# Kernel optimization log

Measured on AMD Instinct MI355X. Metric: run time of the kernel, lower is better.

Reference implementation:

```python
import jax, jax.numpy as jnp
import numpy as np

N = 50000

def setup_inputs() -> dict:
    key = jax.random.key(0)
    ks = jax.random.split(key, 5)
    d, h, E = 128, 512, 800000
    x = jax.random.normal(ks[0], (N, d), dtype=jnp.float32)
    edge_index = jax.random.randint(ks[1], (2, E), 0, N, dtype=jnp.int32)
    eps = jnp.zeros((1, 1), dtype=jnp.float32)
    W1 = jax.random.normal(ks[2], (d, h), dtype=jnp.float32) * (1.0 / np.sqrt(d))
    b1 = jnp.zeros((h,), dtype=jnp.float32)
    W2 = jax.random.normal(ks[3], (h, d), dtype=jnp.float32) * (1.0 / np.sqrt(h))
    b2 = jnp.zeros((d,), dtype=jnp.float32)
    return {"x": x, "edge_index": edge_index, "eps": eps,
            "W1": W1, "b1": b1, "W2": W2, "b2": b2}

def reference(x, edge_index, eps, W1, b1, W2, b2):
    src, dst = edge_index[0], edge_index[1]
    # node -> edge gather (ptens edge subgraph sums both endpoints): [E, d]
    node2edge = x[src] + x[dst]
    # edge -> node gather (sum over incident edges): [N, d]
    nbr = jax.ops.segment_sum(node2edge, src, num_segments=N) + \
          jax.ops.segment_sum(node2edge, dst, num_segments=N)
    # degree correction: subtract deg_i * x_i, leaving sum of neighbor features
    ones = jnp.ones_like(src, dtype=x.dtype)
    deg = jax.ops.segment_sum(ones, src, num_segments=N) + \
          jax.ops.segment_sum(ones, dst, num_segments=N)
    neighbor = nbr - x * deg[:, None]
    # eps-scaled residual then MLP
    out = (1.0 + eps) * x + neighbor
    hmid = jax.nn.relu(out @ W1 + b1)
    return hmid @ W2 + b2
```

## Files before the change

kernel.cpp:

```cpp
#include <hip/hip_runtime.h>

#define MROWS 32
#define FILLK 8
#define WCHUNK 4096

typedef __attribute__((ext_vector_type(8))) short short8v;
typedef __attribute__((ext_vector_type(4))) float f32x4;

__device__ __forceinline__ unsigned short f2bf(float f) {
  unsigned u = __builtin_bit_cast(unsigned, f);
  unsigned r = (u + 0x7fffu + ((u >> 16) & 1u)) >> 16;
  return (unsigned short)r;
}
__device__ __forceinline__ float bf2f(unsigned short s) {
  return __builtin_bit_cast(float, (unsigned)s << 16);
}

__global__ __launch_bounds__(256) void prep_kernel(
    const float* __restrict__ x, const float* __restrict__ W1,
    const float* __restrict__ W2, int* __restrict__ zp,
    unsigned short* __restrict__ xb, short* __restrict__ w1p,
    short* __restrict__ w2p, int N, int zn) {
  const int Z = zn;
  const int X = 16 * N;
  const int grand = Z + X + 131072;
  int i = blockIdx.x * blockDim.x + threadIdx.x;
  int stride = gridDim.x * blockDim.x;
  for (; i < grand; i += stride) {
    if (i < Z) {
      zp[i] = 0;
    } else if (i < Z + X) {
      int t = i - Z;
      const float4* p = (const float4*)(x + (size_t)t * 8);
      float4 q0 = p[0], q1 = p[1];
      short8v s;
      s[0] = (short)f2bf(q0.x); s[1] = (short)f2bf(q0.y);
      s[2] = (short)f2bf(q0.z); s[3] = (short)f2bf(q0.w);
      s[4] = (short)f2bf(q1.x); s[5] = (short)f2bf(q1.y);
      s[6] = (short)f2bf(q1.z); s[7] = (short)f2bf(q1.w);
      *(short8v*)(xb + (size_t)t * 8) = s;
    } else {
      int t = i - Z - X;
      int idx = t & 65535;
      int frag = idx >> 9, rem = idx & 511;
      int lane = rem >> 3, j = rem & 7;
      if (t < 65536) {
        int nt = frag >> 2, ks = frag & 3;
        int k = ks * 32 + (lane >> 4) * 8 + j;
        int c = nt * 16 + (lane & 15);
        w1p[idx] = (short)f2bf(W1[k * 512 + c]);
      } else {
        int nt = frag >> 4, ks = frag & 15;
        int k = ks * 32 + (lane >> 4) * 8 + j;
        int c = nt * 16 + (lane & 15);
        w2p[idx] = (short)f2bf(W2[k * 128 + c]);
      }
    }
  }
}


__global__ __launch_bounds__(256) void bcount_kernel(const int* __restrict__ ei,
    int* __restrict__ bcount, int total, int NB) {
  __shared__ int hist[512];
  for (int i = threadIdx.x; i < 512; i += 256) hist[i] = 0;
  __syncthreads();
  int i = blockIdx.x * blockDim.x + threadIdx.x;
  int stride = gridDim.x * blockDim.x;
  for (; i < total; i += stride) atomicAdd(&hist[((unsigned)ei[i]) >> 7], 1);
  __syncthreads();
  for (int b = threadIdx.x; b < NB; b += 256)
    if (hist[b]) atomicAdd(&bcount[b], hist[b]);
}

__global__ __launch_bounds__(64) void scan_cur_kernel(const int* __restrict__ bcount,
    int* __restrict__ boffs, int* __restrict__ gcursor, int n) {
  int lane = threadIdx.x;
  int carry = 0;
  if (lane == 0) boffs[0] = 0;
  for (int base = 0; base < n; base += 64) {
    int i = base + lane;
    int v0 = (i < n) ? bcount[i] : 0;
    int v = v0;
    #pragma unroll
    for (int off = 1; off < 64; off <<= 1) {
      int t = __shfl_up(v, off, 64);
      if (lane >= off) v += t;
    }
    int incl = v + carry;
    if (i < n) {
      boffs[i + 1] = incl;
      gcursor[i] = incl - v0;
    }
    carry = __shfl(incl, 63, 64);
  }
}

__global__ __launch_bounds__(256) void bwrite_kernel(const int* __restrict__ ei,
    int* __restrict__ gcursor, unsigned* __restrict__ bdata, int E, int NB) {
  __shared__ int hist[512];
  __shared__ int gbase[512];
  const int tid = threadIdx.x;
  const int total = 2 * E;
  const int base0 = blockIdx.x * WCHUNK;
  if (base0 >= total) return;
  const int cnt = min(WCHUNK, total - base0);
  for (int i = tid; i < 512; i += 256) hist[i] = 0;
  __syncthreads();
  for (int k = tid; k < cnt; k += 256)
    atomicAdd(&hist[((unsigned)ei[base0 + k]) >> 7], 1);
  __syncthreads();
  for (int b = tid; b < NB; b += 256) {
    int h = hist[b];
    gbase[b] = h ? atomicAdd(&gcursor[b], h) : 0;
  }
  __syncthreads();
  for (int i = tid; i < 512; i += 256) hist[i] = 0;
  __syncthreads();
  for (int k = tid; k < cnt; k += 256) {
    int i = base0 + k;
    int v = ei[i];
    int other = (i < E) ? ei[i + E] : ei[i - E];
    int b = ((unsigned)v) >> 7;
    int r = atomicAdd(&hist[b], 1);
    bdata[gbase[b] + r] = (((unsigned)(v & 127)) << 16) | (unsigned)other;
  }
}

__global__ __launch_bounds__(256) void bsort_kernel(const unsigned* __restrict__ bdata,
    const int* __restrict__ boffs, unsigned short* __restrict__ adj2,
    int* __restrict__ rowptr, int N, int E2) {
  __shared__ int hist[128];
  __shared__ int loff[129];
  __shared__ int cur[128];
  const int b = blockIdx.x;
  const int beg = boffs[b], end = boffs[b + 1];
  const int tid = threadIdx.x;
  if (tid < 128) hist[tid] = 0;
  __syncthreads();
  for (int p = beg + tid; p < end; p += 256)
    atomicAdd(&hist[bdata[p] >> 16], 1);
  __syncthreads();
  if (tid < 64) {
    int a0 = hist[tid], a1 = hist[tid + 64];
    int v0 = a0;
    #pragma unroll
    for (int off = 1; off < 64; off <<= 1) {
      int t = __shfl_up(v0, off, 64);
      if (tid >= off) v0 += t;
    }
    int tot0 = __shfl(v0, 63, 64);
    int v1 = a1;
    #pragma unroll
    for (int off = 1; off < 64; off <<= 1) {
      int t = __shfl_up(v1, off, 64);
      if (tid >= off) v1 += t;
    }
    loff[tid] = v0 - a0;
    loff[tid + 64] = tot0 + v1 - a1;
    cur[tid] = v0 - a0;
    cur[tid + 64] = tot0 + v1 - a1;
    int n0 = (b << 7) + tid;
    int n1 = n0 + 64;
    if (n0 < N) rowptr[n0] = beg + loff[tid];
    if (n1 < N) rowptr[n1] = beg + loff[tid + 64];
  }
  if (b == 0 && tid == 0) rowptr[N] = E2;
  __syncthreads();
  for (int p = beg + tid; p < end; p += 256) {
    unsigned e = bdata[p];
    int r = atomicAdd(&cur[e >> 16], 1);
    adj2[beg + r] = (unsigned short)(e & 0xFFFFu);
  }
}

__global__ __launch_bounds__(256) void aggb_s_kernel(const unsigned short* __restrict__ xb,
    const float* __restrict__ eps, const int* __restrict__ rowptr,
    const unsigned short* __restrict__ adj2, unsigned short* __restrict__ aggb, int N) {
  int n = blockIdx.x * 16 + (threadIdx.x >> 4);
  if (n >= N) return;
  int lane = threadIdx.x & 15;
  float s = 1.0f + eps[0];
  const unsigned short* lanebase = xb + (size_t)lane * 8;
  short8v own = *(const short8v*)(lanebase + ((size_t)n << 7));
  float accA[8], accB[8];
  #pragma unroll
  for (int j = 0; j < 8; ++j) { accA[j] = bf2f((unsigned short)own[j]) * s; accB[j] = 0.f; }
  int beg = rowptr[n], end = rowptr[n + 1];
  int p = beg;
  for (; p + 4 <= end; p += 4) {
    int j0 = adj2[p + 0];
    int j1 = adj2[p + 1];
    int j2 = adj2[p + 2];
    int j3 = adj2[p + 3];
    short8v v0 = *(const short8v*)(lanebase + ((size_t)j0 << 7));
    short8v v1 = *(const short8v*)(lanebase + ((size_t)j1 << 7));
    short8v v2 = *(const short8v*)(lanebase + ((size_t)j2 << 7));
    short8v v3 = *(const short8v*)(lanebase + ((size_t)j3 << 7));
    #pragma unroll
    for (int j = 0; j < 8; ++j) {
      accA[j] += bf2f((unsigned short)v0[j]) + bf2f((unsigned short)v2[j]);
      accB[j] += bf2f((unsigned short)v1[j]) + bf2f((unsigned short)v3[j]);
    }
  }
  for (; p < end; ++p) {
    int jn = adj2[p];
    short8v v = *(const short8v*)(lanebase + ((size_t)jn << 7));
    #pragma unroll
    for (int j = 0; j < 8; ++j) accA[j] += bf2f((unsigned short)v[j]);
  }
  short8v o;
  #pragma unroll
  for (int j = 0; j < 8; ++j) o[j] = (short)f2bf(accA[j] + accB[j]);
  *(short8v*)(aggb + ((size_t)n << 7) + lane * 8) = o;
}


__global__ __launch_bounds__(256) void count_kernel(const int* __restrict__ ei,
                                                    int* __restrict__ deg, int total) {
  int i = blockIdx.x * blockDim.x + threadIdx.x;
  int stride = gridDim.x * blockDim.x;
  for (; i < total; i += stride) atomicAdd(&deg[ei[i]], 1);
}

__global__ __launch_bounds__(64) void scan_kernel(const int* __restrict__ deg,
                                                  int* __restrict__ rowptr, int n) {
  int lane = threadIdx.x;
  int carry = 0;
  if (lane == 0) rowptr[0] = 0;
  for (int base = 0; base < n; base += 64) {
    int i = base + lane;
    int v = (i < n) ? deg[i] : 0;
    #pragma unroll
    for (int off = 1; off < 64; off <<= 1) {
      int t = __shfl_up(v, off, 64);
      if (lane >= off) v += t;
    }
    int incl = v + carry;
    if (i < n) rowptr[i + 1] = incl;
    carry = __shfl(incl, 63, 64);
  }
}

__global__ __launch_bounds__(256) void chunk_reduce_kernel(const int* __restrict__ deg,
                                                           int* __restrict__ csum, int n) {
  __shared__ int wsum[4];
  int base = blockIdx.x * 1024;
  int tid = threadIdx.x;
  int s = 0;
  #pragma unroll
  for (int j = 0; j < 4; ++j) {
    int i = base + tid * 4 + j;
    if (i < n) s += deg[i];
  }
  #pragma unroll
  for (int off = 1; off < 64; off <<= 1) s += __shfl_xor(s, off, 64);
  if ((tid & 63) == 0) wsum[tid >> 6] = s;
  __syncthreads();
  if (tid == 0) csum[blockIdx.x] = wsum[0] + wsum[1] + wsum[2] + wsum[3];
}

__global__ __launch_bounds__(256) void chunk_scan_c_kernel(const int* __restrict__ deg,
    const int* __restrict__ coffs, int* __restrict__ rowptr,
    int* __restrict__ cursor, int n) {
  __shared__ int wpart[4];
  int b = blockIdx.x;
  int base = b * 1024;
  int tid = threadIdx.x;
  int lane = tid & 63, wv = tid >> 6;
  int v[4], s = 0;
  #pragma unroll
  for (int j = 0; j < 4; ++j) {
    int i = base + tid * 4 + j;
    v[j] = (i < n) ? deg[i] : 0;
    s += v[j];
  }
  int incl = s;
  #pragma unroll
  for (int off = 1; off < 64; off <<= 1) {
    int t = __shfl_up(incl, off, 64);
    if (lane >= off) incl += t;
  }
  if (lane == 63) wpart[wv] = incl;
  __syncthreads();
  int woff = 0;
  for (int k = 0; k < wv; ++k) woff += wpart[k];
  int run = incl - s + woff + coffs[b];
  #pragma unroll
  for (int j = 0; j < 4; ++j) {
    int i = base + tid * 4 + j;
    if (i < n) {
      cursor[i] = run;
      run += v[j];
      rowptr[i + 1] = run;
    }
  }
  if (b == 0 && tid == 0) rowptr[0] = 0;
}

__global__ __launch_bounds__(256) void fill_batch_kernel(const int* __restrict__ ei,
    int* __restrict__ cursor, int* __restrict__ adj, int E) {
  int total = 2 * E;
  int T = gridDim.x * blockDim.x;
  int t = blockIdx.x * blockDim.x + threadIdx.x;
  int vv[FILLK], oo[FILLK], pp[FILLK];
  for (long long base = 0; base < total; base += (long long)T * FILLK) {
    #pragma unroll
    for (int k = 0; k < FILLK; ++k) {
      long long i = base + (long long)k * T + t;
      if (i < total) {
        int ii = (int)i;
        vv[k] = ei[ii];
        oo[k] = (ii < E) ? ei[ii + E] : ei[ii - E];
      } else {
        vv[k] = -1; oo[k] = 0;
      }
    }
    #pragma unroll
    for (int k = 0; k < FILLK; ++k)
      pp[k] = (vv[k] >= 0) ? atomicAdd(&cursor[vv[k]], 1) : 0;
    #pragma unroll
    for (int k = 0; k < FILLK; ++k)
      if (vv[k] >= 0) adj[pp[k]] = oo[k];
  }
}

__global__ __launch_bounds__(256) void aggb_kernel(const unsigned short* __restrict__ xb,
    const float* __restrict__ eps, const int* __restrict__ rowptr,
    const int* __restrict__ adj, unsigned short* __restrict__ aggb, int N) {
  int n = blockIdx.x * 16 + (threadIdx.x >> 4);
  if (n >= N) return;
  int lane = threadIdx.x & 15;
  float s = 1.0f + eps[0];
  const unsigned short* base = xb + (size_t)n * 128 + lane * 8;
  short8v own = *(const short8v*)base;
  float acc[8];
  #pragma unroll
  for (int j = 0; j < 8; ++j) acc[j] = bf2f((unsigned short)own[j]) * s;
  int beg = rowptr[n], end = rowptr[n + 1];
  for (int p = beg; p < end; ++p) {
    int nb = adj[p];
    short8v v = *(const short8v*)(xb + (size_t)nb * 128 + lane * 8);
    #pragma unroll
    for (int j = 0; j < 8; ++j) acc[j] += bf2f((unsigned short)v[j]);
  }
  short8v o;
  #pragma unroll
  for (int j = 0; j < 8; ++j) o[j] = (short)f2bf(acc[j]);
  *(short8v*)(aggb + (size_t)n * 128 + lane * 8) = o;
}


__global__ __launch_bounds__(256) void init_kernel(const float* __restrict__ x,
                                                   const float* __restrict__ eps,
                                                   float* __restrict__ agg, int total4) {
  float scale = 1.0f + eps[0];
  int idx = blockIdx.x * blockDim.x + threadIdx.x;
  int stride = gridDim.x * blockDim.x;
  const float4* x4 = (const float4*)x;
  float4* a4 = (float4*)agg;
  for (int i = idx; i < total4; i += stride) {
    float4 v = x4[i];
    v.x *= scale; v.y *= scale; v.z *= scale; v.w *= scale;
    a4[i] = v;
  }
}

__global__ __launch_bounds__(256) void scatter_kernel(const float* __restrict__ x,
    const int* __restrict__ src, const int* __restrict__ dst,
    float* __restrict__ agg, int E) {
  long long total = (long long)E * 32;
  long long idx = (long long)blockIdx.x * blockDim.x + threadIdx.x;
  long long stride = (long long)gridDim.x * blockDim.x;
  for (; idx < total; idx += stride) {
    int e = (int)(idx >> 5);
    int f4 = (int)(idx & 31);
    int s = src[e], d = dst[e];
    float4 xs = ((const float4*)x)[(size_t)s * 32 + f4];
    float4 xd = ((const float4*)x)[(size_t)d * 32 + f4];
    float* as = agg + (size_t)s * 128 + f4 * 4;
    float* ad = agg + (size_t)d * 128 + f4 * 4;
    atomicAdd(as + 0, xd.x); atomicAdd(as + 1, xd.y);
    atomicAdd(as + 2, xd.z); atomicAdd(as + 3, xd.w);
    atomicAdd(ad + 0, xs.x); atomicAdd(ad + 1, xs.y);
    atomicAdd(ad + 2, xs.z); atomicAdd(ad + 3, xs.w);
  }
}


__global__ __launch_bounds__(256) void mlp_mfma_b_kernel(
    const unsigned short* __restrict__ aggb, const short* __restrict__ w1p,
    const short* __restrict__ w2p, const float* __restrict__ b1,
    const float* __restrict__ b2, float* __restrict__ out, int N) {
  __shared__ short s_h[32 * 512];
  const int tid = threadIdx.x;
  const int w = tid >> 6, l = tid & 63;
  const int l15 = l & 15, lg = l >> 4;
  const int brow = blockIdx.x * 32;

  short8v af[2][4];
  #pragma unroll
  for (int mt = 0; mt < 2; ++mt) {
    int row = brow + mt * 16 + l15;
    #pragma unroll
    for (int ks = 0; ks < 4; ++ks) {
      short8v s = (short8v)(short)0;
      if (row < N)
        s = *(const short8v*)(aggb + (size_t)row * 128 + ks * 32 + lg * 8);
      af[mt][ks] = s;
    }
  }

  f32x4 acc1[2][8];
  #pragma unroll
  for (int nt = 0; nt < 8; ++nt) {
    float bv = b1[(w * 8 + nt) * 16 + l15];
    acc1[0][nt] = (f32x4){bv, bv, bv, bv};
    acc1[1][nt] = (f32x4){bv, bv, bv, bv};
  }
  #pragma unroll
  for (int nt = 0; nt < 8; ++nt) {
    int ntg = w * 8 + nt;
    #pragma unroll
    for (int ks = 0; ks < 4; ++ks) {
      short8v bf = *(const short8v*)(w1p + ((ntg * 4 + ks) << 9) + l * 8);
      acc1[0][nt] = __builtin_amdgcn_mfma_f32_16x16x32_bf16(af[0][ks], bf, acc1[0][nt], 0, 0, 0);
      acc1[1][nt] = __builtin_amdgcn_mfma_f32_16x16x32_bf16(af[1][ks], bf, acc1[1][nt], 0, 0, 0);
    }
  }

  #pragma unroll
  for (int mt = 0; mt < 2; ++mt)
    #pragma unroll
    for (int nt = 0; nt < 8; ++nt) {
      int col = (w * 8 + nt) * 16 + l15;
      #pragma unroll
      for (int reg = 0; reg < 4; ++reg) {
        int row = mt * 16 + lg * 4 + reg;
        float v = fmaxf(acc1[mt][nt][reg], 0.f);
        int byte = (row << 10) + (col << 1);
        byte ^= (row & 7) << 4;
        *(short*)((char*)s_h + byte) = (short)f2bf(v);
      }
    }
  __syncthreads();

  f32x4 acc2[2][2];
  #pragma unroll
  for (int ntl = 0; ntl < 2; ++ntl) {
    float bv = b2[(w * 2 + ntl) * 16 + l15];
    acc2[0][ntl] = (f32x4){bv, bv, bv, bv};
    acc2[1][ntl] = (f32x4){bv, bv, bv, bv};
  }
  #pragma unroll
  for (int ks = 0; ks < 16; ++ks) {
    short8v a2[2];
    #pragma unroll
    for (int mt = 0; mt < 2; ++mt) {
      int row = mt * 16 + l15;
      int byte = (row << 10) + ((ks * 32 + lg * 8) << 1);
      byte ^= (row & 7) << 4;
      a2[mt] = *(short8v*)((char*)s_h + byte);
    }
    #pragma unroll
    for (int ntl = 0; ntl < 2; ++ntl) {
      int ntg = w * 2 + ntl;
      short8v bf = *(const short8v*)(w2p + ((ntg * 16 + ks) << 9) + l * 8);
      acc2[0][ntl] = __builtin_amdgcn_mfma_f32_16x16x32_bf16(a2[0], bf, acc2[0][ntl], 0, 0, 0);
      acc2[1][ntl] = __builtin_amdgcn_mfma_f32_16x16x32_bf16(a2[1], bf, acc2[1][ntl], 0, 0, 0);
    }
  }

  #pragma unroll
  for (int mt = 0; mt < 2; ++mt)
    #pragma unroll
    for (int ntl = 0; ntl < 2; ++ntl)
      #pragma unroll
      for (int reg = 0; reg < 4; ++reg) {
        int row = brow + mt * 16 + lg * 4 + reg;
        if (row < N)
          out[(size_t)row * 128 + (w * 2 + ntl) * 16 + l15] = acc2[mt][ntl][reg];
      }
}


__global__ __launch_bounds__(256) void mlp_kernel(
    const float* agg, const float* __restrict__ W1,
    const float* __restrict__ b1, const float* __restrict__ W2,
    const float* __restrict__ b2, float* out, int N) {
  __shared__ float s_agg[MROWS][128];
  __shared__ float s_h[MROWS][65];
  const int tid = threadIdx.x;
  const int block_row = blockIdx.x * MROWS;

  for (int i = tid; i < MROWS * 32; i += 256) {
    int r = i >> 5, c4 = i & 31;
    if (block_row + r < N)
      ((float4*)&s_agg[r][0])[c4] = ((const float4*)agg)[(size_t)(block_row + r) * 32 + c4];
    else
      ((float4*)&s_agg[r][0])[c4] = make_float4(0.f, 0.f, 0.f, 0.f);
  }
  __syncthreads();

  const int r = tid >> 3;
  const int f0 = (tid & 7) << 4;
  float acc[16];
  #pragma unroll
  for (int j = 0; j < 16; ++j) acc[j] = b2[f0 + j];

  const int hc = tid & 63;
  const int hr0 = tid >> 6;

  for (int h0 = 0; h0 < 512; h0 += 64) {
    float sum[8];
    float bv = b1[h0 + hc];
    #pragma unroll
    for (int j = 0; j < 8; ++j) sum[j] = bv;
    const float* w1col = W1 + h0 + hc;
    #pragma unroll 4
    for (int k = 0; k < 128; ++k) {
      float wv = w1col[(size_t)k * 512];
      #pragma unroll
      for (int j = 0; j < 8; ++j) sum[j] += s_agg[hr0 + (j << 2)][k] * wv;
    }
    __syncthreads();
    #pragma unroll
    for (int j = 0; j < 8; ++j) s_h[hr0 + (j << 2)][hc] = fmaxf(sum[j], 0.f);
    __syncthreads();

    for (int hcc = 0; hcc < 64; ++hcc) {
      float hv = s_h[r][hcc];
      const float4* w2p = (const float4*)(W2 + (size_t)(h0 + hcc) * 128 + f0);
      float4 w0 = w2p[0], w1v = w2p[1], w2v = w2p[2], w3v = w2p[3];
      acc[0]  += hv * w0.x;  acc[1]  += hv * w0.y;  acc[2]  += hv * w0.z;  acc[3]  += hv * w0.w;
      acc[4]  += hv * w1v.x; acc[5]  += hv * w1v.y; acc[6]  += hv * w1v.z; acc[7]  += hv * w1v.w;
      acc[8]  += hv * w2v.x; acc[9]  += hv * w2v.y; acc[10] += hv * w2v.z; acc[11] += hv * w2v.w;
      acc[12] += hv * w3v.x; acc[13] += hv * w3v.y; acc[14] += hv * w3v.z; acc[15] += hv * w3v.w;
    }
  }

  if (block_row + r < N) {
    float4* op = (float4*)(out + (size_t)(block_row + r) * 128 + f0);
    op[0] = make_float4(acc[0],  acc[1],  acc[2],  acc[3]);
    op[1] = make_float4(acc[4],  acc[5],  acc[6],  acc[7]);
    op[2] = make_float4(acc[8],  acc[9],  acc[10], acc[11]);
    op[3] = make_float4(acc[12], acc[13], acc[14], acc[15]);
  }
}

extern "C" void kernel_launch(void* const* d_in, const int* in_sizes, int n_in,
                              void* d_out, int out_size, void* d_ws, size_t ws_size,
                              hipStream_t stream) {
  const float* x   = (const float*)d_in[0];
  const int*   ei  = (const int*)d_in[1];
  const float* eps = (const float*)d_in[2];
  const float* W1  = (const float*)d_in[3];
  const float* b1  = (const float*)d_in[4];
  const float* W2  = (const float*)d_in[5];
  const float* b2  = (const float*)d_in[6];
  float* out = (float*)d_out;

  const int N = in_sizes[0] / 128;
  const int E = in_sizes[1] / 2;
  const int nChunks = (N + 1023) / 1024;
  const int NB = (N + 127) >> 7;
  int mblocks = (N + MROWS - 1) / MROWS;

  size_t wp_bytes = 2u * 65536u * sizeof(short);
  size_t xb_bytes = ((size_t)N * 128 * sizeof(short) + 15) & ~(size_t)15;

  size_t bt_ints = (size_t)2 * NB + (NB + 1) + (size_t)(N + 1) + (size_t)2 * E + (size_t)(E + 1);
  size_t bt_al = ((bt_ints * sizeof(int)) + 15) & ~(size_t)15;
  size_t need_bt = bt_al + wp_bytes + 2 * xb_bytes;

  size_t csr_ints = (size_t)(3 * N + 1 + 2 * E) + (size_t)(2 * nChunks + 1);
  size_t csr_al = ((csr_ints * sizeof(int)) + 15) & ~(size_t)15;
  size_t need_t1 = csr_al + wp_bytes;
  size_t need_t2 = need_t1 + 2 * xb_bytes;

  if (N <= 65536 && ws_size >= need_bt) {
    int* bcount  = (int*)d_ws;
    int* gcursor = bcount + NB;
    int* boffs   = gcursor + NB;
    int* rowptr  = boffs + NB + 1;
    unsigned* bdata = (unsigned*)(rowptr + N + 1);
    unsigned short* adj2 = (unsigned short*)(bdata + 2 * E);
    short* w1p  = (short*)((char*)d_ws + bt_al);
    short* w2p  = w1p + 65536;
    unsigned short* xb   = (unsigned short*)((char*)d_ws + bt_al + wp_bytes);
    unsigned short* aggb = (unsigned short*)((char*)d_ws + bt_al + wp_bytes + xb_bytes);

    prep_kernel<<<2048, 256, 0, stream>>>(x, W1, W2, bcount, xb, w1p, w2p, N, NB);
    bcount_kernel<<<256, 256, 0, stream>>>(ei, bcount, 2 * E, NB);
    scan_cur_kernel<<<1, 64, 0, stream>>>(bcount, boffs, gcursor, NB);
    int wblocks = (2 * E + WCHUNK - 1) / WCHUNK;
    bwrite_kernel<<<wblocks, 256, 0, stream>>>(ei, gcursor, bdata, E, NB);
    bsort_kernel<<<NB, 256, 0, stream>>>(bdata, boffs, adj2, rowptr, N, 2 * E);
    aggb_s_kernel<<<(N + 15) / 16, 256, 0, stream>>>(xb, eps, rowptr, adj2, aggb, N);
    mlp_mfma_b_kernel<<<mblocks, 256, 0, stream>>>(aggb, w1p, w2p, b1, b2, out, N);
  } else if (ws_size >= need_t2) {
    int* deg    = (int*)d_ws;
    int* cursor = deg + N;
    int* rowptr = cursor + N;
    int* adj    = rowptr + (N + 1);
    int* csum   = adj + 2 * E;
    int* coffs  = csum + nChunks;
    short* w1p  = (short*)((char*)d_ws + csr_al);
    short* w2p  = w1p + 65536;
    unsigned short* xb   = (unsigned short*)((char*)d_ws + need_t1);
    unsigned short* aggb = (unsigned short*)((char*)d_ws + need_t1 + xb_bytes);

    prep_kernel<<<2048, 256, 0, stream>>>(x, W1, W2, deg, xb, w1p, w2p, N, 2 * N);
    count_kernel<<<4096, 256, 0, stream>>>(ei, deg, 2 * E);
    chunk_reduce_kernel<<<nChunks, 256, 0, stream>>>(deg, csum, N);
    scan_kernel<<<1, 64, 0, stream>>>(csum, coffs, nChunks);
    chunk_scan_c_kernel<<<nChunks, 256, 0, stream>>>(deg, coffs, rowptr, cursor, N);
    int fblocks = (2 * E + 256 * FILLK - 1) / (256 * FILLK);
    fill_batch_kernel<<<fblocks, 256, 0, stream>>>(ei, cursor, adj, E);
    aggb_kernel<<<(N + 15) / 16, 256, 0, stream>>>(xb, eps, rowptr, adj, aggb, N);
    mlp_mfma_b_kernel<<<mblocks, 256, 0, stream>>>(aggb, w1p, w2p, b1, b2, out, N);
  } else {
    init_kernel<<<2048, 256, 0, stream>>>(x, eps, out, N * 32);
    scatter_kernel<<<4096, 256, 0, stream>>>(x, ei, ei + E, out, E);
    mlp_kernel<<<mblocks, 256, 0, stream>>>(out, W1, b1, W2, b2, out, N);
  }
}
```

Baseline: 162.8 us.

## Fuse neighbor aggregation into MFMA MLP kernel via shared-memory staging

```diff
diff --git a/kernel.cpp b/kernel.cpp
--- a/kernel.cpp
+++ b/kernel.cpp
@@ -174,45 +174,151 @@
   }
 }
 
-__global__ __launch_bounds__(256) void aggb_s_kernel(const unsigned short* __restrict__ xb,
-    const float* __restrict__ eps, const int* __restrict__ rowptr,
-    const unsigned short* __restrict__ adj2, unsigned short* __restrict__ aggb, int N) {
-  int n = blockIdx.x * 16 + (threadIdx.x >> 4);
-  if (n >= N) return;
-  int lane = threadIdx.x & 15;
-  float s = 1.0f + eps[0];
-  const unsigned short* lanebase = xb + (size_t)lane * 8;
-  short8v own = *(const short8v*)(lanebase + ((size_t)n << 7));
-  float accA[8], accB[8];
-  #pragma unroll
-  for (int j = 0; j < 8; ++j) { accA[j] = bf2f((unsigned short)own[j]) * s; accB[j] = 0.f; }
-  int beg = rowptr[n], end = rowptr[n + 1];
-  int p = beg;
-  for (; p + 4 <= end; p += 4) {
-    int j0 = adj2[p + 0];
-    int j1 = adj2[p + 1];
-    int j2 = adj2[p + 2];
-    int j3 = adj2[p + 3];
-    short8v v0 = *(const short8v*)(lanebase + ((size_t)j0 << 7));
-    short8v v1 = *(const short8v*)(lanebase + ((size_t)j1 << 7));
-    short8v v2 = *(const short8v*)(lanebase + ((size_t)j2 << 7));
-    short8v v3 = *(const short8v*)(lanebase + ((size_t)j3 << 7));
-    #pragma unroll
-    for (int j = 0; j < 8; ++j) {
-      accA[j] += bf2f((unsigned short)v0[j]) + bf2f((unsigned short)v2[j]);
-      accB[j] += bf2f((unsigned short)v1[j]) + bf2f((unsigned short)v3[j]);
-    }
-  }
-  for (; p < end; ++p) {
-    int jn = adj2[p];
-    short8v v = *(const short8v*)(lanebase + ((size_t)jn << 7));
-    #pragma unroll
-    for (int j = 0; j < 8; ++j) accA[j] += bf2f((unsigned short)v[j]);
-  }
-  short8v o;
-  #pragma unroll
-  for (int j = 0; j < 8; ++j) o[j] = (short)f2bf(accA[j] + accB[j]);
-  *(short8v*)(aggb + ((size_t)n << 7) + lane * 8) = o;
+__global__ __launch_bounds__(256) void agg_mlp_fused_kernel(
+    const unsigned short* __restrict__ xb, const float* __restrict__ eps,
+    const int* __restrict__ rowptr, const unsigned short* __restrict__ adj2,
+    const short* __restrict__ w1p, const short* __restrict__ w2p,
+    const float* __restrict__ b1, const float* __restrict__ b2,
+    float* __restrict__ out, int N) {
+  __shared__ short s_agg[32 * 128];
+  __shared__ short s_h[32 * 512];
+  const int tid = threadIdx.x;
+  const int brow = blockIdx.x * 32;
+
+  {
+    const int lane16 = tid & 15;
+    const unsigned short* lanebase = xb + (size_t)lane16 * 8;
+    float s = 1.0f + eps[0];
+    #pragma unroll
+    for (int half = 0; half < 2; ++half) {
+      int r = half * 16 + (tid >> 4);
+      int n = brow + r;
+      float accA[8], accB[8];
+      #pragma unroll
+      for (int j = 0; j < 8; ++j) { accA[j] = 0.f; accB[j] = 0.f; }
+      if (n < N) {
+        short8v own = *(const short8v*)(lanebase + ((size_t)n << 7));
+        #pragma unroll
+        for (int j = 0; j < 8; ++j) accA[j] = bf2f((unsigned short)own[j]) * s;
+        int beg = rowptr[n], end = rowptr[n + 1];
+        int p = beg;
+        for (; p + 4 <= end; p += 4) {
+          int j0 = adj2[p + 0];
+          int j1 = adj2[p + 1];
+          int j2 = adj2[p + 2];
+          int j3 = adj2[p + 3];
+          short8v v0 = *(const short8v*)(lanebase + ((size_t)j0 << 7));
+          short8v v1 = *(const short8v*)(lanebase + ((size_t)j1 << 7));
+          short8v v2 = *(const short8v*)(lanebase + ((size_t)j2 << 7));
+          short8v v3 = *(const short8v*)(lanebase + ((size_t)j3 << 7));
+          #pragma unroll
+          for (int j = 0; j < 8; ++j) {
+            accA[j] += bf2f((unsigned short)v0[j]) + bf2f((unsigned short)v2[j]);
+            accB[j] += bf2f((unsigned short)v1[j]) + bf2f((unsigned short)v3[j]);
+          }
+        }
+        for (; p < end; ++p) {
+          int jn = adj2[p];
+          short8v v = *(const short8v*)(lanebase + ((size_t)jn << 7));
+          #pragma unroll
+          for (int j = 0; j < 8; ++j) accA[j] += bf2f((unsigned short)v[j]);
+        }
+      }
+      short8v o;
+      #pragma unroll
+      for (int j = 0; j < 8; ++j) o[j] = (short)f2bf(accA[j] + accB[j]);
+      int byte = (r << 8) + (lane16 << 4);
+      byte ^= (r & 7) << 4;
+      *(short8v*)((char*)s_agg + byte) = o;
+    }
+  }
+  __syncthreads();
+
+  const int w = tid >> 6, l = tid & 63;
+  const int l15 = l & 15, lg = l >> 4;
+
+  short8v af[2][4];
+  #pragma unroll
+  for (int mt = 0; mt < 2; ++mt) {
+    int row = mt * 16 + l15;
+    #pragma unroll
+    for (int ks = 0; ks < 4; ++ks) {
+      int byte = (row << 8) + ((ks * 32 + lg * 8) << 1);
+      byte ^= (row & 7) << 4;
+      af[mt][ks] = *(short8v*)((char*)s_agg + byte);
+    }
+  }
+
+  f32x4 acc1[2][8];
+  #pragma unroll
+  for (int nt = 0; nt < 8; ++nt) {
+    float bv = b1[(w * 8 + nt) * 16 + l15];
+    acc1[0][nt] = (f32x4){bv, bv, bv, bv};
+    acc1[1][nt] = (f32x4){bv, bv, bv, bv};
+  }
+  #pragma unroll
+  for (int nt = 0; nt < 8; ++nt) {
+    int ntg = w * 8 + nt;
+    #pragma unroll
+    for (int ks = 0; ks < 4; ++ks) {
+      short8v bf = *(const short8v*)(w1p + ((ntg * 4 + ks) << 9) + l * 8);
+      acc1[0][nt] = __builtin_amdgcn_mfma_f32_16x16x32_bf16(af[0][ks], bf, acc1[0][nt], 0, 0, 0);
+      acc1[1][nt] = __builtin_amdgcn_mfma_f32_16x16x32_bf16(af[1][ks], bf, acc1[1][nt], 0, 0, 0);
+    }
+  }
+
+  #pragma unroll
+  for (int mt = 0; mt < 2; ++mt)
+    #pragma unroll
+    for (int nt = 0; nt < 8; ++nt) {
+      int col = (w * 8 + nt) * 16 + l15;
+      #pragma unroll
+      for (int reg = 0; reg < 4; ++reg) {
+        int row = mt * 16 + lg * 4 + reg;
+        float v = fmaxf(acc1[mt][nt][reg], 0.f);
+        int byte = (row << 10) + (col << 1);
+        byte ^= (row & 7) << 4;
+        *(short*)((char*)s_h + byte) = (short)f2bf(v);
+      }
+    }
+  __syncthreads();
+
+  f32x4 acc2[2][2];
+  #pragma unroll
+  for (int ntl = 0; ntl < 2; ++ntl) {
+    float bv = b2[(w * 2 + ntl) * 16 + l15];
+    acc2[0][ntl] = (f32x4){bv, bv, bv, bv};
+    acc2[1][ntl] = (f32x4){bv, bv, bv, bv};
+  }
+  #pragma unroll
+  for (int ks = 0; ks < 16; ++ks) {
+    short8v a2[2];
+    #pragma unroll
+    for (int mt = 0; mt < 2; ++mt) {
+      int row = mt * 16 + l15;
+      int byte = (row << 10) + ((ks * 32 + lg * 8) << 1);
+      byte ^= (row & 7) << 4;
+      a2[mt] = *(short8v*)((char*)s_h + byte);
+    }
+    #pragma unroll
+    for (int ntl = 0; ntl < 2; ++ntl) {
+      int ntg = w * 2 + ntl;
+      short8v bf = *(const short8v*)(w2p + ((ntg * 16 + ks) << 9) + l * 8);
+      acc2[0][ntl] = __builtin_amdgcn_mfma_f32_16x16x32_bf16(a2[0], bf, acc2[0][ntl], 0, 0, 0);
+      acc2[1][ntl] = __builtin_amdgcn_mfma_f32_16x16x32_bf16(a2[1], bf, acc2[1][ntl], 0, 0, 0);
+    }
+  }
+
+  #pragma unroll
+  for (int mt = 0; mt < 2; ++mt)
+    #pragma unroll
+    for (int ntl = 0; ntl < 2; ++ntl)
+      #pragma unroll
+      for (int reg = 0; reg < 4; ++reg) {
+        int row = brow + mt * 16 + lg * 4 + reg;
+        if (row < N)
+          out[(size_t)row * 128 + (w * 2 + ntl) * 16 + l15] = acc2[mt][ntl][reg];
+      }
 }
 
 
@@ -588,7 +694,6 @@
     short* w1p  = (short*)((char*)d_ws + bt_al);
     short* w2p  = w1p + 65536;
     unsigned short* xb   = (unsigned short*)((char*)d_ws + bt_al + wp_bytes);
-    unsigned short* aggb = (unsigned short*)((char*)d_ws + bt_al + wp_bytes + xb_bytes);
 
     prep_kernel<<<2048, 256, 0, stream>>>(x, W1, W2, bcount, xb, w1p, w2p, N, NB);
     bcount_kernel<<<256, 256, 0, stream>>>(ei, bcount, 2 * E, NB);
@@ -596,8 +701,8 @@
     int wblocks = (2 * E + WCHUNK - 1) / WCHUNK;
     bwrite_kernel<<<wblocks, 256, 0, stream>>>(ei, gcursor, bdata, E, NB);
     bsort_kernel<<<NB, 256, 0, stream>>>(bdata, boffs, adj2, rowptr, N, 2 * E);
-    aggb_s_kernel<<<(N + 15) / 16, 256, 0, stream>>>(xb, eps, rowptr, adj2, aggb, N);
-    mlp_mfma_b_kernel<<<mblocks, 256, 0, stream>>>(aggb, w1p, w2p, b1, b2, out, N);
+    agg_mlp_fused_kernel<<<mblocks, 256, 0, stream>>>(xb, eps, rowptr, adj2,
+                                                      w1p, w2p, b1, b2, out, N);
   } else if (ws_size >= need_t2) {
     int* deg    = (int*)d_ws;
     int* cursor = deg + N;
```

After: 165.9 us. No clear change (+1.9%).

## Fuse bucket histogram into prep kernel and unroll gather loop by eight

Applied to the files above, without the earlier changes.

```diff
diff --git a/kernel.cpp b/kernel.cpp
--- a/kernel.cpp
+++ b/kernel.cpp
@@ -14,6 +14,56 @@
 }
 __device__ __forceinline__ float bf2f(unsigned short s) {
   return __builtin_bit_cast(float, (unsigned)s << 16);
+}
+
+__global__ __launch_bounds__(256) void prep_b_kernel(
+    const float* __restrict__ x, const float* __restrict__ W1,
+    const float* __restrict__ W2, const int* __restrict__ ei,
+    int* __restrict__ bcount, unsigned short* __restrict__ xb,
+    short* __restrict__ w1p, short* __restrict__ w2p, int N, int E, int NB) {
+  __shared__ int hist[512];
+  for (int i = threadIdx.x; i < 512; i += 256) hist[i] = 0;
+  __syncthreads();
+  const int X = 16 * N;
+  const int grand = X + 131072;
+  int i = blockIdx.x * blockDim.x + threadIdx.x;
+  int stride = gridDim.x * blockDim.x;
+  for (; i < grand; i += stride) {
+    if (i < X) {
+      const float4* p = (const float4*)(x + (size_t)i * 8);
+      float4 q0 = p[0], q1 = p[1];
+      short8v s;
+      s[0] = (short)f2bf(q0.x); s[1] = (short)f2bf(q0.y);
+      s[2] = (short)f2bf(q0.z); s[3] = (short)f2bf(q0.w);
+      s[4] = (short)f2bf(q1.x); s[5] = (short)f2bf(q1.y);
+      s[6] = (short)f2bf(q1.z); s[7] = (short)f2bf(q1.w);
+      *(short8v*)(xb + (size_t)i * 8) = s;
+    } else {
+      int t = i - X;
+      int idx = t & 65535;
+      int frag = idx >> 9, rem = idx & 511;
+      int lane = rem >> 3, j = rem & 7;
+      if (t < 65536) {
+        int nt = frag >> 2, ks = frag & 3;
+        int k = ks * 32 + (lane >> 4) * 8 + j;
+        int c = nt * 16 + (lane & 15);
+        w1p[idx] = (short)f2bf(W1[k * 512 + c]);
+      } else {
+        int nt = frag >> 4, ks = frag & 15;
+        int k = ks * 32 + (lane >> 4) * 8 + j;
+        int c = nt * 16 + (lane & 15);
+        w2p[idx] = (short)f2bf(W2[k * 128 + c]);
+      }
+    }
+  }
+  if (blockIdx.x < 256) {
+    int total = 2 * E;
+    for (int k = blockIdx.x * 256 + threadIdx.x; k < total; k += 256 * 256)
+      atomicAdd(&hist[((unsigned)ei[k]) >> 7], 1);
+    __syncthreads();
+    for (int b = threadIdx.x; b < NB; b += 256)
+      if (hist[b]) atomicAdd(&bcount[b], hist[b]);
+  }
 }
 
 __global__ __launch_bounds__(256) void prep_kernel(
@@ -188,11 +238,27 @@
   for (int j = 0; j < 8; ++j) { accA[j] = bf2f((unsigned short)own[j]) * s; accB[j] = 0.f; }
   int beg = rowptr[n], end = rowptr[n + 1];
   int p = beg;
+  for (; p + 8 <= end; p += 8) {
+    int j0 = adj2[p + 0], j1 = adj2[p + 1], j2 = adj2[p + 2], j3 = adj2[p + 3];
+    int j4 = adj2[p + 4], j5 = adj2[p + 5], j6 = adj2[p + 6], j7 = adj2[p + 7];
+    short8v v0 = *(const short8v*)(lanebase + ((size_t)j0 << 7));
+    short8v v1 = *(const short8v*)(lanebase + ((size_t)j1 << 7));
+    short8v v2 = *(const short8v*)(lanebase + ((size_t)j2 << 7));
+    short8v v3 = *(const short8v*)(lanebase + ((size_t)j3 << 7));
+    short8v v4 = *(const short8v*)(lanebase + ((size_t)j4 << 7));
+    short8v v5 = *(const short8v*)(lanebase + ((size_t)j5 << 7));
+    short8v v6 = *(const short8v*)(lanebase + ((size_t)j6 << 7));
+    short8v v7 = *(const short8v*)(lanebase + ((size_t)j7 << 7));
+    #pragma unroll
+    for (int j = 0; j < 8; ++j) {
+      accA[j] += (bf2f((unsigned short)v0[j]) + bf2f((unsigned short)v2[j]))
+               + (bf2f((unsigned short)v4[j]) + bf2f((unsigned short)v6[j]));
+      accB[j] += (bf2f((unsigned short)v1[j]) + bf2f((unsigned short)v3[j]))
+               + (bf2f((unsigned short)v5[j]) + bf2f((unsigned short)v7[j]));
+    }
+  }
   for (; p + 4 <= end; p += 4) {
-    int j0 = adj2[p + 0];
-    int j1 = adj2[p + 1];
-    int j2 = adj2[p + 2];
-    int j3 = adj2[p + 3];
+    int j0 = adj2[p + 0], j1 = adj2[p + 1], j2 = adj2[p + 2], j3 = adj2[p + 3];
     short8v v0 = *(const short8v*)(lanebase + ((size_t)j0 << 7));
     short8v v1 = *(const short8v*)(lanebase + ((size_t)j1 << 7));
     short8v v2 = *(const short8v*)(lanebase + ((size_t)j2 << 7));
@@ -590,8 +656,8 @@
     unsigned short* xb   = (unsigned short*)((char*)d_ws + bt_al + wp_bytes);
     unsigned short* aggb = (unsigned short*)((char*)d_ws + bt_al + wp_bytes + xb_bytes);
 
-    prep_kernel<<<2048, 256, 0, stream>>>(x, W1, W2, bcount, xb, w1p, w2p, N, NB);
-    bcount_kernel<<<256, 256, 0, stream>>>(ei, bcount, 2 * E, NB);
+    hipMemsetAsync(bcount, 0, (size_t)NB * sizeof(int), stream);
+    prep_b_kernel<<<2048, 256, 0, stream>>>(x, W1, W2, ei, bcount, xb, w1p, w2p, N, E, NB);
     scan_cur_kernel<<<1, 64, 0, stream>>>(bcount, boffs, gcursor, NB);
     int wblocks = (2 * E + WCHUNK - 1) / WCHUNK;
     bwrite_kernel<<<wblocks, 256, 0, stream>>>(ei, gcursor, bdata, E, NB);
```

Measured after the change: 164.6 us. Within noise of the previous version (+1.1%).
